# Kernel tuning notes

Measured on AMD Instinct MI355X. Metric: run time of the kernel, lower is better.

## Reference

```python
import jax, jax.numpy as jnp
import numpy as np


def setup_inputs() -> dict:
    key = jax.random.key(0)
    k1, k2, k3, k4 = jax.random.split(key, 4)
    N = 100000          # n_users + n_items nodes
    E = 1600000         # nonzeros in normalized adjacency (avg degree 16)
    D = 64              # embedding dim
    edge_row = jnp.sort(jax.random.randint(k1, (E,), 0, N, dtype=jnp.int32))
    edge_col = jax.random.randint(k2, (E,), 0, N, dtype=jnp.int32)
    edge_val = jax.random.uniform(k3, (E,), dtype=jnp.float32)
    embeds = jax.random.normal(k4, (N, D), dtype=jnp.float32)
    return {
        "edge_row": edge_row,
        "edge_col": edge_col,
        "edge_val": edge_val,
        "embeds": embeds,
        "num_nodes": N,
    }


def reference(edge_row, edge_col, edge_val, embeds, num_nodes):
    # out = A @ embeds, A given in COO: A[row[e], col[e]] = val[e]
    gathered = edge_val[:, None] * embeds[edge_col]        # [E, D]
    out = jax.ops.segment_sum(gathered, edge_row, num_segments=num_nodes)  # [N, D]
    return out
```

## Files before the change

### kernel.cpp

```cpp
#include <hip/hip_runtime.h>


#define GCN_D 64

typedef float f4 __attribute__((ext_vector_type(4)));

__global__ __launch_bounds__(256) void prep_kernel(
    const float* __restrict__ embeds,
    unsigned char* __restrict__ ebq,
    float* __restrict__ scale,
    int quant_blocks,
    const int* __restrict__ edge_row, int* __restrict__ row_ptr, int E, int N)
{
    if ((int)blockIdx.x < quant_blocks) {
        const int t   = blockIdx.x * blockDim.x + threadIdx.x;
        const int row = t >> 3;
        if (row >= N) return;
        const int l8 = (threadIdx.x & 7) * 8;

        const f4 a = __builtin_nontemporal_load(
            (const f4*)(embeds + (size_t)row * GCN_D + l8));
        const f4 b = __builtin_nontemporal_load(
            (const f4*)(embeds + (size_t)row * GCN_D + l8 + 4));

        float m = fmaxf(fmaxf(fmaxf(fabsf(a.x), fabsf(a.y)),
                              fmaxf(fabsf(a.z), fabsf(a.w))),
                        fmaxf(fmaxf(fabsf(b.x), fabsf(b.y)),
                              fmaxf(fabsf(b.z), fabsf(b.w))));
        m = fmaxf(m, __shfl_xor(m, 1));
        m = fmaxf(m, __shfl_xor(m, 2));
        m = fmaxf(m, __shfl_xor(m, 4));

        const float inv = (m > 0.f) ? 127.f / m : 0.f;
        const int q0 = (int)rintf(fminf(fmaxf(a.x * inv, -127.f), 127.f)) + 128;
        const int q1 = (int)rintf(fminf(fmaxf(a.y * inv, -127.f), 127.f)) + 128;
        const int q2 = (int)rintf(fminf(fmaxf(a.z * inv, -127.f), 127.f)) + 128;
        const int q3 = (int)rintf(fminf(fmaxf(a.w * inv, -127.f), 127.f)) + 128;
        const int q4 = (int)rintf(fminf(fmaxf(b.x * inv, -127.f), 127.f)) + 128;
        const int q5 = (int)rintf(fminf(fmaxf(b.y * inv, -127.f), 127.f)) + 128;
        const int q6 = (int)rintf(fminf(fmaxf(b.z * inv, -127.f), 127.f)) + 128;
        const int q7 = (int)rintf(fminf(fmaxf(b.w * inv, -127.f), 127.f)) + 128;

        unsigned int p0 =
            (unsigned)q0 | ((unsigned)q1 << 8) | ((unsigned)q2 << 16) | ((unsigned)q3 << 24);
        unsigned int p1 =
            (unsigned)q4 | ((unsigned)q5 << 8) | ((unsigned)q6 << 16) | ((unsigned)q7 << 24);

        unsigned int* dst = (unsigned int*)(ebq + (size_t)row * GCN_D + l8);
        dst[0] = p0;
        dst[1] = p1;
        if ((threadIdx.x & 7) == 0) scale[row] = m * (1.f / 127.f);
    } else {
        const int e = (blockIdx.x - quant_blocks) * blockDim.x + threadIdx.x;
        if (e >= E) return;
        const int r    = edge_row[e];
        const int prev = (e == 0) ? -1 : edge_row[e - 1];
        for (int k = prev + 1; k <= r; ++k) row_ptr[k] = e;
        if (e == E - 1)
            for (int k = r + 1; k <= N; ++k) row_ptr[k] = E;
    }
}

__global__ __launch_bounds__(256) void gcn_row_q8_kernel(
    const int* __restrict__ row_ptr,
    const int* __restrict__ edge_col,
    const float* __restrict__ edge_val,
    const unsigned char* __restrict__ ebq,
    const float* __restrict__ scale,
    float* __restrict__ out,
    int N)
{
    const int tid = blockIdx.x * blockDim.x + threadIdx.x;
    const int row = tid >> 4;
    if (row >= N) return;
    const int db = (threadIdx.x & 15) * 4;

    const int p0 = row_ptr[row];
    const int p1 = row_ptr[row + 1];

    f4    acc  = (f4)0.0f;
    float wsum = 0.0f;
    int k = p0;

    for (; k + 7 < p1; k += 8) {
        int   c[8];
        float v[8];
        #pragma unroll
        for (int j = 0; j < 8; ++j) { c[j] = edge_col[k + j]; v[j] = edge_val[k + j]; }
        unsigned int g[8];
        float        s[8];
        #pragma unroll
        for (int j = 0; j < 8; ++j) {
            g[j] = *(const unsigned int*)(ebq + (size_t)c[j] * GCN_D + db);
            s[j] = scale[c[j]];
        }
        #pragma unroll
        for (int j = 0; j < 8; ++j) {
            const float w = v[j] * s[j];
            acc.x += w * (float)( g[j]        & 0xffu);
            acc.y += w * (float)((g[j] >> 8)  & 0xffu);
            acc.z += w * (float)((g[j] >> 16) & 0xffu);
            acc.w += w * (float)( g[j] >> 24);
            wsum  += w;
        }
    }
    if (k + 3 < p1) {
        int   c[4];
        float v[4];
        #pragma unroll
        for (int j = 0; j < 4; ++j) { c[j] = edge_col[k + j]; v[j] = edge_val[k + j]; }
        unsigned int g[4];
        float        s[4];
        #pragma unroll
        for (int j = 0; j < 4; ++j) {
            g[j] = *(const unsigned int*)(ebq + (size_t)c[j] * GCN_D + db);
            s[j] = scale[c[j]];
        }
        #pragma unroll
        for (int j = 0; j < 4; ++j) {
            const float w = v[j] * s[j];
            acc.x += w * (float)( g[j]        & 0xffu);
            acc.y += w * (float)((g[j] >> 8)  & 0xffu);
            acc.z += w * (float)((g[j] >> 16) & 0xffu);
            acc.w += w * (float)( g[j] >> 24);
            wsum  += w;
        }
        k += 4;
    }
    for (; k < p1; ++k) {
        const int c = edge_col[k];
        const unsigned int g = *(const unsigned int*)(ebq + (size_t)c * GCN_D + db);
        const float w = edge_val[k] * scale[c];
        acc.x += w * (float)( g        & 0xffu);
        acc.y += w * (float)((g >> 8)  & 0xffu);
        acc.z += w * (float)((g >> 16) & 0xffu);
        acc.w += w * (float)( g >> 24);
        wsum  += w;
    }

    acc = acc - 128.0f * wsum;

    __builtin_nontemporal_store(acc, (f4*)(out + (size_t)row * GCN_D + db));
}

extern "C" void kernel_launch(void* const* d_in, const int* in_sizes, int n_in,
                              void* d_out, int out_size, void* d_ws, size_t ws_size,
                              hipStream_t stream) {
    const int*   edge_row = (const int*)d_in[0];
    const int*   edge_col = (const int*)d_in[1];
    const float* edge_val = (const float*)d_in[2];
    const float* embeds   = (const float*)d_in[3];
    float*       out      = (float*)d_out;

    const int E = in_sizes[0];
    const int N = out_size / GCN_D;

    int* row_ptr = (int*)d_ws;
    const size_t sc_off = (((size_t)(N + 1) * 4) + 255) & ~(size_t)255;
    float* scale = (float*)((char*)d_ws + sc_off);
    const size_t q_off = ((sc_off + (size_t)N * 4) + 255) & ~(size_t)255;
    unsigned char* ebq = (unsigned char*)d_ws + q_off;

    const int quant_blocks = (N * 8 + 255) / 256;
    const int rp_blocks    = (E + 255) / 256;
    prep_kernel<<<quant_blocks + rp_blocks, 256, 0, stream>>>(
        embeds, ebq, scale, quant_blocks, edge_row, row_ptr, E, N);

    const int row_blocks = (N * 16 + 255) / 256;
    gcn_row_q8_kernel<<<row_blocks, 256, 0, stream>>>(
        row_ptr, edge_col, edge_val, ebq, scale, out, N);
}
```

Baseline: 126.7 us.

## Switch SpMM to edge-chunked merge-path style with atomic boundary flushes

Replaces row-per-16-thread SpMM with fixed 32-edge chunks per 16-thread group, so every group does equal work regardless of row degree. Rows entirely inside a chunk are written with a plain store, and rows that span chunk boundaries are combined with float atomics. This requires a memset of the output first. Loads are vectorized and software-pipelined (double-buffered by 4 edges). The change adds the memset cost, atomic traffic on boundary rows and an extra edge_row stream, and makes results depend on atomic ordering.

```diff
diff --git a/kernel.cpp b/kernel.cpp
--- a/kernel.cpp
+++ b/kernel.cpp
@@ -4,6 +4,7 @@
 #define GCN_D 64
 
 typedef float f4 __attribute__((ext_vector_type(4)));
+typedef int   i4 __attribute__((ext_vector_type(4)));
 
 __global__ __launch_bounds__(256) void prep_kernel(
     const float* __restrict__ embeds,
@@ -61,86 +62,100 @@
     }
 }
 
-__global__ __launch_bounds__(256) void gcn_row_q8_kernel(
+__device__ __forceinline__ void q8_fma4(unsigned int g, float w, f4& acc) {
+    acc.x += w * (float)( g        & 0xffu);
+    acc.y += w * (float)((g >> 8)  & 0xffu);
+    acc.z += w * (float)((g >> 16) & 0xffu);
+    acc.w += w * (float)( g >> 24);
+}
+
+#define CHUNK 32
+
+__global__ __launch_bounds__(256) void gcn_edge_q8_kernel(
+    const int* __restrict__ edge_row,
     const int* __restrict__ row_ptr,
     const int* __restrict__ edge_col,
     const float* __restrict__ edge_val,
     const unsigned char* __restrict__ ebq,
     const float* __restrict__ scale,
     float* __restrict__ out,
-    int N)
+    int E)
 {
     const int tid = blockIdx.x * blockDim.x + threadIdx.x;
-    const int row = tid >> 4;
-    if (row >= N) return;
+    const int grp = tid >> 4;
+    const int k0  = grp * CHUNK;
+    if (k0 >= E) return;
+    const int k1 = min(k0 + CHUNK, E);
     const int db = (threadIdx.x & 15) * 4;
 
-    const int p0 = row_ptr[row];
-    const int p1 = row_ptr[row + 1];
+    int   r   = edge_row[k0];
+    f4    acc = (f4)0.0f;
+    float ws  = 0.0f;
 
-    f4    acc  = (f4)0.0f;
-    float wsum = 0.0f;
-    int k = p0;
+    auto flush = [&](int rr, f4 a, float w) {
+        a = a - 128.0f * w;
+        float* dst = out + (size_t)rr * GCN_D + db;
+        const bool interior = (row_ptr[rr] >= k0) && (row_ptr[rr + 1] <= k1);
+        if (interior) {
+            __builtin_nontemporal_store(a, (f4*)dst);
+        } else {
+            atomicAdd(dst + 0, a.x);
+            atomicAdd(dst + 1, a.y);
+            atomicAdd(dst + 2, a.z);
+            atomicAdd(dst + 3, a.w);
+        }
+    };
 
-    for (; k + 7 < p1; k += 8) {
-        int   c[8];
-        float v[8];
-        #pragma unroll
-        for (int j = 0; j < 8; ++j) { c[j] = edge_col[k + j]; v[j] = edge_val[k + j]; }
-        unsigned int g[8];
-        float        s[8];
-        #pragma unroll
-        for (int j = 0; j < 8; ++j) {
-            g[j] = *(const unsigned int*)(ebq + (size_t)c[j] * GCN_D + db);
-            s[j] = scale[c[j]];
-        }
-        #pragma unroll
-        for (int j = 0; j < 8; ++j) {
-            const float w = v[j] * s[j];
-            acc.x += w * (float)( g[j]        & 0xffu);
-            acc.y += w * (float)((g[j] >> 8)  & 0xffu);
-            acc.z += w * (float)((g[j] >> 16) & 0xffu);
-            acc.w += w * (float)( g[j] >> 24);
-            wsum  += w;
+    int k = k0;
+    if (k + 3 < k1) {
+        i4 rrA, cA; f4 vA; unsigned gA0, gA1, gA2, gA3; float sA0, sA1, sA2, sA3;
+        rrA = *(const i4*)(edge_row + k);
+        cA  = *(const i4*)(edge_col + k);
+        vA  = *(const f4*)(edge_val + k);
+        gA0 = *(const unsigned*)(ebq + (size_t)cA.x * GCN_D + db); sA0 = scale[cA.x];
+        gA1 = *(const unsigned*)(ebq + (size_t)cA.y * GCN_D + db); sA1 = scale[cA.y];
+        gA2 = *(const unsigned*)(ebq + (size_t)cA.z * GCN_D + db); sA2 = scale[cA.z];
+        gA3 = *(const unsigned*)(ebq + (size_t)cA.w * GCN_D + db); sA3 = scale[cA.w];
+
+        for (; k + 3 < k1; k += 4) {
+            i4 rrB, cB; f4 vB; unsigned gB0, gB1, gB2, gB3; float sB0, sB1, sB2, sB3;
+            const bool more = (k + 7 < k1);
+            if (more) {
+                rrB = *(const i4*)(edge_row + k + 4);
+                cB  = *(const i4*)(edge_col + k + 4);
+                vB  = *(const f4*)(edge_val + k + 4);
+                gB0 = *(const unsigned*)(ebq + (size_t)cB.x * GCN_D + db); sB0 = scale[cB.x];
+                gB1 = *(const unsigned*)(ebq + (size_t)cB.y * GCN_D + db); sB1 = scale[cB.y];
+                gB2 = *(const unsigned*)(ebq + (size_t)cB.z * GCN_D + db); sB2 = scale[cB.z];
+                gB3 = *(const unsigned*)(ebq + (size_t)cB.w * GCN_D + db); sB3 = scale[cB.w];
+            }
+
+            if (rrA.x != r) { flush(r, acc, ws); acc = (f4)0.0f; ws = 0.0f; r = rrA.x; }
+            { const float w = vA.x * sA0; q8_fma4(gA0, w, acc); ws += w; }
+            if (rrA.y != r) { flush(r, acc, ws); acc = (f4)0.0f; ws = 0.0f; r = rrA.y; }
+            { const float w = vA.y * sA1; q8_fma4(gA1, w, acc); ws += w; }
+            if (rrA.z != r) { flush(r, acc, ws); acc = (f4)0.0f; ws = 0.0f; r = rrA.z; }
+            { const float w = vA.z * sA2; q8_fma4(gA2, w, acc); ws += w; }
+            if (rrA.w != r) { flush(r, acc, ws); acc = (f4)0.0f; ws = 0.0f; r = rrA.w; }
+            { const float w = vA.w * sA3; q8_fma4(gA3, w, acc); ws += w; }
+
+            if (more) {
+                rrA = rrB; cA = cB; vA = vB;
+                gA0 = gB0; gA1 = gB1; gA2 = gB2; gA3 = gB3;
+                sA0 = sB0; sA1 = sB1; sA2 = sB2; sA3 = sB3;
+            }
         }
     }
-    if (k + 3 < p1) {
-        int   c[4];
-        float v[4];
-        #pragma unroll
-        for (int j = 0; j < 4; ++j) { c[j] = edge_col[k + j]; v[j] = edge_val[k + j]; }
-        unsigned int g[4];
-        float        s[4];
-        #pragma unroll
-        for (int j = 0; j < 4; ++j) {
-            g[j] = *(const unsigned int*)(ebq + (size_t)c[j] * GCN_D + db);
-            s[j] = scale[c[j]];
-        }
-        #pragma unroll
-        for (int j = 0; j < 4; ++j) {
-            const float w = v[j] * s[j];
-            acc.x += w * (float)( g[j]        & 0xffu);
-            acc.y += w * (float)((g[j] >> 8)  & 0xffu);
-            acc.z += w * (float)((g[j] >> 16) & 0xffu);
-            acc.w += w * (float)( g[j] >> 24);
-            wsum  += w;
-        }
-        k += 4;
+    for (; k < k1; ++k) {
+        const int rj = edge_row[k];
+        if (rj != r) { flush(r, acc, ws); acc = (f4)0.0f; ws = 0.0f; r = rj; }
+        const int c = edge_col[k];
+        const unsigned g = *(const unsigned*)(ebq + (size_t)c * GCN_D + db);
+        const float w = edge_val[k] * scale[c];
+        q8_fma4(g, w, acc);
+        ws += w;
     }
-    for (; k < p1; ++k) {
-        const int c = edge_col[k];
-        const unsigned int g = *(const unsigned int*)(ebq + (size_t)c * GCN_D + db);
-        const float w = edge_val[k] * scale[c];
-        acc.x += w * (float)( g        & 0xffu);
-        acc.y += w * (float)((g >> 8)  & 0xffu);
-        acc.z += w * (float)((g >> 16) & 0xffu);
-        acc.w += w * (float)( g >> 24);
-        wsum  += w;
-    }
-
-    acc = acc - 128.0f * wsum;
-
-    __builtin_nontemporal_store(acc, (f4*)(out + (size_t)row * GCN_D + db));
+    flush(r, acc, ws);
 }
 
 extern "C" void kernel_launch(void* const* d_in, const int* in_sizes, int n_in,
@@ -161,12 +176,15 @@
     const size_t q_off = ((sc_off + (size_t)N * 4) + 255) & ~(size_t)255;
     unsigned char* ebq = (unsigned char*)d_ws + q_off;
 
+    hipMemsetAsync(d_out, 0, (size_t)out_size * sizeof(float), stream);
+
     const int quant_blocks = (N * 8 + 255) / 256;
     const int rp_blocks    = (E + 255) / 256;
     prep_kernel<<<quant_blocks + rp_blocks, 256, 0, stream>>>(
         embeds, ebq, scale, quant_blocks, edge_row, row_ptr, E, N);
 
-    const int row_blocks = (N * 16 + 255) / 256;
-    gcn_row_q8_kernel<<<row_blocks, 256, 0, stream>>>(
-        row_ptr, edge_col, edge_val, ebq, scale, out, N);
+    const int groups       = (E + CHUNK - 1) / CHUNK;
+    const int gather_blocks = (groups * 16 + 255) / 256;
+    gcn_edge_q8_kernel<<<gather_blocks, 256, 0, stream>>>(
+        edge_row, row_ptr, edge_col, edge_val, ebq, scale, out, E);
 }
```

After: 193.2 us. 1.52x slower.

## Assign one full wavefront per row with byte-wide gathers and uniform indices

Applied to the files above, without the earlier changes.

Restructures the SpMM gather so each 64-lane wavefront handles one row, with each lane owning one byte-quantized dimension instead of 16 lanes each owning four. The row index is made wave-uniform via readfirstlane so edge indices, values and scales can be fetched as scalar loads rather than redundantly per lane. This trades 4x more threads and narrower per-lane memory accesses for fewer redundant index loads and simpler per-thread arithmetic.

```diff
diff --git a/kernel.cpp b/kernel.cpp
--- a/kernel.cpp
+++ b/kernel.cpp
@@ -61,7 +61,7 @@
     }
 }
 
-__global__ __launch_bounds__(256) void gcn_row_q8_kernel(
+__global__ __launch_bounds__(256) void gcn_wave_q8_kernel(
     const int* __restrict__ row_ptr,
     const int* __restrict__ edge_col,
     const float* __restrict__ edge_val,
@@ -70,16 +70,16 @@
     float* __restrict__ out,
     int N)
 {
-    const int tid = blockIdx.x * blockDim.x + threadIdx.x;
-    const int row = tid >> 4;
+    const int row = __builtin_amdgcn_readfirstlane(
+        (int)((blockIdx.x * blockDim.x + threadIdx.x) >> 6));
     if (row >= N) return;
-    const int db = (threadIdx.x & 15) * 4;
+    const int lane = (int)(threadIdx.x & 63);
 
     const int p0 = row_ptr[row];
     const int p1 = row_ptr[row + 1];
 
-    f4    acc  = (f4)0.0f;
-    float wsum = 0.0f;
+    float acc = 0.0f;
+    float ws  = 0.0f;
     int k = p0;
 
     for (; k + 7 < p1; k += 8) {
@@ -87,21 +87,18 @@
         float v[8];
         #pragma unroll
         for (int j = 0; j < 8; ++j) { c[j] = edge_col[k + j]; v[j] = edge_val[k + j]; }
-        unsigned int g[8];
-        float        s[8];
+        unsigned g[8];
+        float    s[8];
         #pragma unroll
         for (int j = 0; j < 8; ++j) {
-            g[j] = *(const unsigned int*)(ebq + (size_t)c[j] * GCN_D + db);
+            g[j] = ebq[(size_t)c[j] * GCN_D + lane];
             s[j] = scale[c[j]];
         }
         #pragma unroll
         for (int j = 0; j < 8; ++j) {
             const float w = v[j] * s[j];
-            acc.x += w * (float)( g[j]        & 0xffu);
-            acc.y += w * (float)((g[j] >> 8)  & 0xffu);
-            acc.z += w * (float)((g[j] >> 16) & 0xffu);
-            acc.w += w * (float)( g[j] >> 24);
-            wsum  += w;
+            acc = fmaf(w, (float)g[j], acc);
+            ws += w;
         }
     }
     if (k + 3 < p1) {
@@ -109,38 +106,31 @@
         float v[4];
         #pragma unroll
         for (int j = 0; j < 4; ++j) { c[j] = edge_col[k + j]; v[j] = edge_val[k + j]; }
-        unsigned int g[4];
-        float        s[4];
+        unsigned g[4];
+        float    s[4];
         #pragma unroll
         for (int j = 0; j < 4; ++j) {
-            g[j] = *(const unsigned int*)(ebq + (size_t)c[j] * GCN_D + db);
+            g[j] = ebq[(size_t)c[j] * GCN_D + lane];
             s[j] = scale[c[j]];
         }
         #pragma unroll
         for (int j = 0; j < 4; ++j) {
             const float w = v[j] * s[j];
-            acc.x += w * (float)( g[j]        & 0xffu);
-            acc.y += w * (float)((g[j] >> 8)  & 0xffu);
-            acc.z += w * (float)((g[j] >> 16) & 0xffu);
-            acc.w += w * (float)( g[j] >> 24);
-            wsum  += w;
+            acc = fmaf(w, (float)g[j], acc);
+            ws += w;
         }
         k += 4;
     }
     for (; k < p1; ++k) {
         const int c = edge_col[k];
-        const unsigned int g = *(const unsigned int*)(ebq + (size_t)c * GCN_D + db);
+        const unsigned g = ebq[(size_t)c * GCN_D + lane];
         const float w = edge_val[k] * scale[c];
-        acc.x += w * (float)( g        & 0xffu);
-        acc.y += w * (float)((g >> 8)  & 0xffu);
-        acc.z += w * (float)((g >> 16) & 0xffu);
-        acc.w += w * (float)( g >> 24);
-        wsum  += w;
+        acc = fmaf(w, (float)g, acc);
+        ws += w;
     }
 
-    acc = acc - 128.0f * wsum;
-
-    __builtin_nontemporal_store(acc, (f4*)(out + (size_t)row * GCN_D + db));
+    __builtin_nontemporal_store(acc - 128.0f * ws,
+                                out + (size_t)row * GCN_D + lane);
 }
 
 extern "C" void kernel_launch(void* const* d_in, const int* in_sizes, int n_in,
@@ -166,7 +156,7 @@
     prep_kernel<<<quant_blocks + rp_blocks, 256, 0, stream>>>(
         embeds, ebq, scale, quant_blocks, edge_row, row_ptr, E, N);
 
-    const int row_blocks = (N * 16 + 255) / 256;
-    gcn_row_q8_kernel<<<row_blocks, 256, 0, stream>>>(
+    const int gather_blocks = (N * 64 + 255) / 256;
+    gcn_wave_q8_kernel<<<gather_blocks, 256, 0, stream>>>(
         row_ptr, edge_col, edge_val, ebq, scale, out, N);
 }
```

New measurement: 156.4 us. +23.4%, slower.

## Prefold scale into packed edge weights and double-buffer gathers in SpMM

Applied to the files above, without the earlier changes.

Splits the prep kernel into a quantization kernel and an edge kernel. The edge kernel builds row_ptr and also writes packed (col, val*scale) int2 pairs, so the main kernel no longer does a dependent scale gather per edge. The main SpMM loop now double-buffers batches of 8 edges, padding the tail with masked loads, so the next batch's gathers are issued before the current batch is accumulated. In exchange it adds a kernel launch and a serial dependency between the two prep kernels, an extra 8E-byte write and read, and higher register pressure.

```diff
diff --git a/kernel.cpp b/kernel.cpp
--- a/kernel.cpp
+++ b/kernel.cpp
@@ -5,68 +5,84 @@
 
 typedef float f4 __attribute__((ext_vector_type(4)));
 
-__global__ __launch_bounds__(256) void prep_kernel(
+__global__ __launch_bounds__(256) void quant_kernel(
     const float* __restrict__ embeds,
     unsigned char* __restrict__ ebq,
     float* __restrict__ scale,
-    int quant_blocks,
-    const int* __restrict__ edge_row, int* __restrict__ row_ptr, int E, int N)
+    int N)
 {
-    if ((int)blockIdx.x < quant_blocks) {
-        const int t   = blockIdx.x * blockDim.x + threadIdx.x;
-        const int row = t >> 3;
-        if (row >= N) return;
-        const int l8 = (threadIdx.x & 7) * 8;
+    const int t   = blockIdx.x * blockDim.x + threadIdx.x;
+    const int row = t >> 3;
+    if (row >= N) return;
+    const int l8 = (threadIdx.x & 7) * 8;
 
-        const f4 a = __builtin_nontemporal_load(
-            (const f4*)(embeds + (size_t)row * GCN_D + l8));
-        const f4 b = __builtin_nontemporal_load(
-            (const f4*)(embeds + (size_t)row * GCN_D + l8 + 4));
+    const f4 a = __builtin_nontemporal_load(
+        (const f4*)(embeds + (size_t)row * GCN_D + l8));
+    const f4 b = __builtin_nontemporal_load(
+        (const f4*)(embeds + (size_t)row * GCN_D + l8 + 4));
 
-        float m = fmaxf(fmaxf(fmaxf(fabsf(a.x), fabsf(a.y)),
-                              fmaxf(fabsf(a.z), fabsf(a.w))),
-                        fmaxf(fmaxf(fabsf(b.x), fabsf(b.y)),
-                              fmaxf(fabsf(b.z), fabsf(b.w))));
-        m = fmaxf(m, __shfl_xor(m, 1));
-        m = fmaxf(m, __shfl_xor(m, 2));
-        m = fmaxf(m, __shfl_xor(m, 4));
+    float m = fmaxf(fmaxf(fmaxf(fabsf(a.x), fabsf(a.y)),
+                          fmaxf(fabsf(a.z), fabsf(a.w))),
+                    fmaxf(fmaxf(fabsf(b.x), fabsf(b.y)),
+                          fmaxf(fabsf(b.z), fabsf(b.w))));
+    m = fmaxf(m, __shfl_xor(m, 1));
+    m = fmaxf(m, __shfl_xor(m, 2));
+    m = fmaxf(m, __shfl_xor(m, 4));
 
-        const float inv = (m > 0.f) ? 127.f / m : 0.f;
-        const int q0 = (int)rintf(fminf(fmaxf(a.x * inv, -127.f), 127.f)) + 128;
-        const int q1 = (int)rintf(fminf(fmaxf(a.y * inv, -127.f), 127.f)) + 128;
-        const int q2 = (int)rintf(fminf(fmaxf(a.z * inv, -127.f), 127.f)) + 128;
-        const int q3 = (int)rintf(fminf(fmaxf(a.w * inv, -127.f), 127.f)) + 128;
-        const int q4 = (int)rintf(fminf(fmaxf(b.x * inv, -127.f), 127.f)) + 128;
-        const int q5 = (int)rintf(fminf(fmaxf(b.y * inv, -127.f), 127.f)) + 128;
-        const int q6 = (int)rintf(fminf(fmaxf(b.z * inv, -127.f), 127.f)) + 128;
-        const int q7 = (int)rintf(fminf(fmaxf(b.w * inv, -127.f), 127.f)) + 128;
+    const float inv = (m > 0.f) ? 127.f / m : 0.f;
+    const int q0 = (int)rintf(fminf(fmaxf(a.x * inv, -127.f), 127.f)) + 128;
+    const int q1 = (int)rintf(fminf(fmaxf(a.y * inv, -127.f), 127.f)) + 128;
+    const int q2 = (int)rintf(fminf(fmaxf(a.z * inv, -127.f), 127.f)) + 128;
+    const int q3 = (int)rintf(fminf(fmaxf(a.w * inv, -127.f), 127.f)) + 128;
+    const int q4 = (int)rintf(fminf(fmaxf(b.x * inv, -127.f), 127.f)) + 128;
+    const int q5 = (int)rintf(fminf(fmaxf(b.y * inv, -127.f), 127.f)) + 128;
+    const int q6 = (int)rintf(fminf(fmaxf(b.z * inv, -127.f), 127.f)) + 128;
+    const int q7 = (int)rintf(fminf(fmaxf(b.w * inv, -127.f), 127.f)) + 128;
 
-        unsigned int p0 =
-            (unsigned)q0 | ((unsigned)q1 << 8) | ((unsigned)q2 << 16) | ((unsigned)q3 << 24);
-        unsigned int p1 =
-            (unsigned)q4 | ((unsigned)q5 << 8) | ((unsigned)q6 << 16) | ((unsigned)q7 << 24);
+    unsigned int p0 =
+        (unsigned)q0 | ((unsigned)q1 << 8) | ((unsigned)q2 << 16) | ((unsigned)q3 << 24);
+    unsigned int p1 =
+        (unsigned)q4 | ((unsigned)q5 << 8) | ((unsigned)q6 << 16) | ((unsigned)q7 << 24);
 
-        unsigned int* dst = (unsigned int*)(ebq + (size_t)row * GCN_D + l8);
-        dst[0] = p0;
-        dst[1] = p1;
-        if ((threadIdx.x & 7) == 0) scale[row] = m * (1.f / 127.f);
-    } else {
-        const int e = (blockIdx.x - quant_blocks) * blockDim.x + threadIdx.x;
-        if (e >= E) return;
-        const int r    = edge_row[e];
-        const int prev = (e == 0) ? -1 : edge_row[e - 1];
-        for (int k = prev + 1; k <= r; ++k) row_ptr[k] = e;
-        if (e == E - 1)
-            for (int k = r + 1; k <= N; ++k) row_ptr[k] = E;
-    }
+    unsigned int* dst = (unsigned int*)(ebq + (size_t)row * GCN_D + l8);
+    dst[0] = p0;
+    dst[1] = p1;
+    if ((threadIdx.x & 7) == 0) scale[row] = m * (1.f / 127.f);
+}
+
+__global__ __launch_bounds__(256) void edge_kernel(
+    const int* __restrict__ edge_row,
+    const int* __restrict__ edge_col,
+    const float* __restrict__ edge_val,
+    const float* __restrict__ scale,
+    int* __restrict__ row_ptr,
+    int2* __restrict__ pw,
+    int E, int N)
+{
+    const int e = blockIdx.x * blockDim.x + threadIdx.x;
+    if (e >= E) return;
+    const int r    = edge_row[e];
+    const int prev = (e == 0) ? -1 : edge_row[e - 1];
+    for (int k = prev + 1; k <= r; ++k) row_ptr[k] = e;
+    if (e == E - 1)
+        for (int k = r + 1; k <= N; ++k) row_ptr[k] = E;
+
+    const int   c = edge_col[e];
+    const float w = edge_val[e] * scale[c];
+    pw[e] = make_int2(c, __float_as_int(w));
+}
+
+__device__ __forceinline__ void q8_fma4(unsigned int g, float w, f4& acc) {
+    acc.x += w * (float)( g        & 0xffu);
+    acc.y += w * (float)((g >> 8)  & 0xffu);
+    acc.z += w * (float)((g >> 16) & 0xffu);
+    acc.w += w * (float)( g >> 24);
 }
 
 __global__ __launch_bounds__(256) void gcn_row_q8_kernel(
     const int* __restrict__ row_ptr,
-    const int* __restrict__ edge_col,
-    const float* __restrict__ edge_val,
+    const int2* __restrict__ pw,
     const unsigned char* __restrict__ ebq,
-    const float* __restrict__ scale,
     float* __restrict__ out,
     int N)
 {
@@ -78,68 +94,55 @@
     const int p0 = row_ptr[row];
     const int p1 = row_ptr[row + 1];
 
-    f4    acc  = (f4)0.0f;
-    float wsum = 0.0f;
-    int k = p0;
+    f4    acc = (f4)0.0f;
+    float ws  = 0.0f;
 
-    for (; k + 7 < p1; k += 8) {
-        int   c[8];
-        float v[8];
-        #pragma unroll
-        for (int j = 0; j < 8; ++j) { c[j] = edge_col[k + j]; v[j] = edge_val[k + j]; }
-        unsigned int g[8];
-        float        s[8];
-        #pragma unroll
-        for (int j = 0; j < 8; ++j) {
-            g[j] = *(const unsigned int*)(ebq + (size_t)c[j] * GCN_D + db);
-            s[j] = scale[c[j]];
+    if (p1 > p0) {
+        const int nb = (p1 - p0 + 7) >> 3;
+        int k = p0;
+
+        int      cA[8], cB[8];
+        float    wA[8], wB[8];
+        unsigned gA[8], gB[8];
+
+        auto LOAD = [&](int kk, int* c, float* w, unsigned* g) {
+            #pragma unroll
+            for (int j = 0; j < 8; ++j) {
+                const int idx = (kk + j < p1) ? (kk + j) : (p1 - 1);
+                const int2 t  = pw[idx];
+                c[j] = t.x;
+                w[j] = (kk + j < p1) ? __int_as_float(t.y) : 0.0f;
+            }
+            #pragma unroll
+            for (int j = 0; j < 8; ++j)
+                g[j] = *(const unsigned*)(ebq + (size_t)c[j] * GCN_D + db);
+        };
+        auto COMP = [&](const float* w, const unsigned* g) {
+            #pragma unroll
+            for (int j = 0; j < 8; ++j) {
+                q8_fma4(g[j], w[j], acc);
+                ws += w[j];
+            }
+        };
+
+        LOAD(k, cA, wA, gA); k += 8;
+        int b = 1;
+        for (; b + 1 < nb; b += 2) {
+            LOAD(k, cB, wB, gB); k += 8;
+            COMP(wA, gA);
+            LOAD(k, cA, wA, gA); k += 8;
+            COMP(wB, gB);
         }
-        #pragma unroll
-        for (int j = 0; j < 8; ++j) {
-            const float w = v[j] * s[j];
-            acc.x += w * (float)( g[j]        & 0xffu);
-            acc.y += w * (float)((g[j] >> 8)  & 0xffu);
-            acc.z += w * (float)((g[j] >> 16) & 0xffu);
-            acc.w += w * (float)( g[j] >> 24);
-            wsum  += w;
+        if (b < nb) {
+            LOAD(k, cB, wB, gB);
+            COMP(wA, gA);
+            COMP(wB, gB);
+        } else {
+            COMP(wA, gA);
         }
     }
-    if (k + 3 < p1) {
-        int   c[4];
-        float v[4];
-        #pragma unroll
-        for (int j = 0; j < 4; ++j) { c[j] = edge_col[k + j]; v[j] = edge_val[k + j]; }
-        unsigned int g[4];
-        float        s[4];
-        #pragma unroll
-        for (int j = 0; j < 4; ++j) {
-            g[j] = *(const unsigned int*)(ebq + (size_t)c[j] * GCN_D + db);
-            s[j] = scale[c[j]];
-        }
-        #pragma unroll
-        for (int j = 0; j < 4; ++j) {
-            const float w = v[j] * s[j];
-            acc.x += w * (float)( g[j]        & 0xffu);
-            acc.y += w * (float)((g[j] >> 8)  & 0xffu);
-            acc.z += w * (float)((g[j] >> 16) & 0xffu);
-            acc.w += w * (float)( g[j] >> 24);
-            wsum  += w;
-        }
-        k += 4;
-    }
-    for (; k < p1; ++k) {
-        const int c = edge_col[k];
-        const unsigned int g = *(const unsigned int*)(ebq + (size_t)c * GCN_D + db);
-        const float w = edge_val[k] * scale[c];
-        acc.x += w * (float)( g        & 0xffu);
-        acc.y += w * (float)((g >> 8)  & 0xffu);
-        acc.z += w * (float)((g >> 16) & 0xffu);
-        acc.w += w * (float)( g >> 24);
-        wsum  += w;
-    }
 
-    acc = acc - 128.0f * wsum;
-
+    acc = acc - 128.0f * ws;
     __builtin_nontemporal_store(acc, (f4*)(out + (size_t)row * GCN_D + db));
 }
 
@@ -158,15 +161,19 @@
     int* row_ptr = (int*)d_ws;
     const size_t sc_off = (((size_t)(N + 1) * 4) + 255) & ~(size_t)255;
     float* scale = (float*)((char*)d_ws + sc_off);
-    const size_t q_off = ((sc_off + (size_t)N * 4) + 255) & ~(size_t)255;
+    const size_t pw_off = ((sc_off + (size_t)N * 4) + 255) & ~(size_t)255;
+    int2* pw = (int2*)((char*)d_ws + pw_off);
+    const size_t q_off = ((pw_off + (size_t)E * 8) + 255) & ~(size_t)255;
     unsigned char* ebq = (unsigned char*)d_ws + q_off;
 
     const int quant_blocks = (N * 8 + 255) / 256;
-    const int rp_blocks    = (E + 255) / 256;
-    prep_kernel<<<quant_blocks + rp_blocks, 256, 0, stream>>>(
-        embeds, ebq, scale, quant_blocks, edge_row, row_ptr, E, N);
+    quant_kernel<<<quant_blocks, 256, 0, stream>>>(embeds, ebq, scale, N);
+
+    const int edge_blocks = (E + 255) / 256;
+    edge_kernel<<<edge_blocks, 256, 0, stream>>>(
+        edge_row, edge_col, edge_val, scale, row_ptr, pw, E, N);
 
     const int row_blocks = (N * 16 + 255) / 256;
     gcn_row_q8_kernel<<<row_blocks, 256, 0, stream>>>(
-        row_ptr, edge_col, edge_val, ebq, scale, out, N);
+        row_ptr, pw, ebq, out, N);
 }
```

Result: slower. 139.6 us (+10.2%).
